# Kernel tuning notes

Measured on AMD Instinct MI355X. Metric: run time of the kernel, lower is better.

The kernel has to match this reference:

```python
import jax, jax.numpy as jnp
import numpy as np

B, R, N, M, K = 4, 4, 4096, 64, 3
F_NUM = 512
KN = K * N


def _block(x, Ws, bs):
    """SO-Net PointResNet: 1x1 convs + ReLU; last layer sees concat(input, hidden)."""
    h = x
    for W, b in zip(Ws[:-1], bs[:-1]):
        h = jax.nn.relu(jnp.einsum('oc,bcn->bon', W, h) + b[None, :, None])
    h = jnp.concatenate([x, h], axis=1)
    return jax.nn.relu(jnp.einsum('oc,bcn->bon', Ws[-1], h) + bs[-1][None, :, None])


def _forward(x, intensity, node, node_knn_I, fpW, fpB, gpW, gpB):
    # --- som.query_topk: k nearest SOM nodes per point ---
    xd = jax.lax.stop_gradient(x)
    dist = jnp.sum((xd[:, :, :, None] - node[:, :, None, :]) ** 2, axis=1)      # B,N,M
    _, topk = jax.lax.top_k(-dist, K)                                           # B,N,K
    min_idx = topk.transpose(0, 2, 1).reshape(B, KN)                            # B,KN (k copies stacked)
    mask = jax.nn.one_hot(min_idx, M, dtype=jnp.float32)                        # B,KN,M
    mask_row_max = jnp.max(mask, axis=1) > 0                                    # B,M  node has >=1 point
    mask_row_sum = jnp.sum(mask, axis=1)                                        # B,M  points per node

    x_stack = jnp.tile(x, (1, 1, K))                                            # B,2,KN
    cluster_mean = jnp.einsum('bcn,bnm->bcm', jax.lax.stop_gradient(x_stack), mask) \
                   / (mask_row_sum[:, None, :] + 1e-5)                          # B,2,M (detached)

    # --- rotation group (2x2 rotations at angles 2*pi*r/R) ---
    theta = 2.0 * jnp.pi * jnp.arange(R, dtype=jnp.float32) / R
    c, s = jnp.cos(theta), jnp.sin(theta)
    rot = jnp.stack([jnp.stack([c, -s], -1), jnp.stack([s, c], -1)], -2)        # R,2,2

    x_rot = jnp.einsum('rij,bjn->brin', rot, x_stack)                           # B,R,2,KN
    node_rot = jnp.einsum('rij,bjm->brim', rot, cluster_mean)                   # B,R,2,M
    centers = jnp.take_along_axis(node_rot, min_idx[:, None, None, :], axis=3)  # B,R,2,KN
    x_dec = jax.lax.stop_gradient(x_rot - centers).reshape(B * R, 2, KN)

    # --- first PointResNet over all B*R rotation copies ---
    feat = _block(x_dec, fpW, fpB)                                              # BR,128,KN

    # --- index_max scatter-max per SOM cluster (value of argmax == segment max) ---
    seg = jnp.tile(min_idx[:, None, :], (1, R, 1)).reshape(B * R, KN)
    segmax = jax.vmap(lambda f, sgi: jax.ops.segment_max(f.T, sgi, num_segments=M).T)(feat, seg)
    rowmax = jnp.tile(mask_row_max[:, None, :], (1, R, 1)).reshape(B * R, M)
    pooled = jnp.where(rowmax[:, None, :], segmax, feat[:, :, 0:1])             # BR,128,M (empty -> gather idx 0)

    # --- final PointResNet over SOM nodes, then max over nodes and rotations ---
    g_in = jnp.concatenate([node_rot.reshape(B * R, 2, M), pooled], axis=1)     # BR,130,M
    out = _block(g_in, gpW, gpB)                                                # BR,F,M
    return out.reshape(B, R, F_NUM, M).max(axis=3).max(axis=1)                  # B,F


def setup_inputs() -> dict:
    key = jax.random.key(0)
    ks = jax.random.split(key, 24)
    d = {}
    d['x'] = jax.random.normal(ks[0], (B, 2, N), jnp.float32)
    d['intensity'] = jax.random.uniform(ks[1], (B, 1, N), jnp.float32)
    d['node'] = jax.random.normal(ks[2], (B, 2, M), jnp.float32)
    d['node_knn_I'] = jax.random.randint(ks[3], (B, M, 1), 0, M)
    dims_fp = [(64, 2), (64, 64), (128, 64), (128, 130)]      # PointResNet(2,[64,64,128,128])
    dims_gp = [(256, 130), (256, 256), (512, 256), (F_NUM, 642)]  # PointResNet(130,[256,256,512,F])
    i = 4
    for name, dims in (('fp', dims_fp), ('gp', dims_gp)):
        for j, (o, ci) in enumerate(dims):
            d[f'{name}_W{j}'] = jax.random.normal(ks[i], (o, ci), jnp.float32) / np.sqrt(ci).astype(np.float32)
            d[f'{name}_b{j}'] = jnp.zeros((o,), jnp.float32)
            i += 1
    return d


def reference(x, intensity, node, node_knn_I,
              fp_W0, fp_b0, fp_W1, fp_b1, fp_W2, fp_b2, fp_W3, fp_b3,
              gp_W0, gp_b0, gp_W1, gp_b1, gp_W2, gp_b2, gp_W3, gp_b3):
    return _forward(x, intensity, node, node_knn_I,
                    [fp_W0, fp_W1, fp_W2, fp_W3], [fp_b0, fp_b1, fp_b2, fp_b3],
                    [gp_W0, gp_W1, gp_W2, gp_W3], [gp_b0, gp_b1, gp_b2, gp_b3])
```

## Files before the change

### kernel.cpp

```cpp
#include <hip/hip_runtime.h>
#include <stdint.h>

#define BB 4
#define RR 4
#define NN 4096
#define MM 64
#define KK 3
#define KNN 12288
#define BRR 16
#define FF 512

#define W_FPW1 0
#define W_FPW2 4096
#define W_FPW3 12288
#define W_GPW0 28928
#define W_GPW1 62208
#define W_GPW2 127744
#define W_GPW3 258816
#define W_FPB1 587520
#define W_FPB2 587584
#define W_FPB3 587712
#define W_GPB0 587840
#define W_GPB1 588096
#define W_GPB2 588352
#define W_GPB3 588864
#define W_FPB0 589376
#define W_FPW0 589440
#define W_TOT  589568

typedef short bf16x8 __attribute__((ext_vector_type(8)));
typedef float f32x4 __attribute__((ext_vector_type(4)));

__device__ __forceinline__ float bf2f(unsigned int u) {
  union { unsigned int i; float f; } v; v.i = u << 16; return v.f;
}
__device__ __forceinline__ unsigned short f2bf(float f) {
  union { float f; unsigned int i; } v; v.f = f;
  unsigned int x = v.i;
  return (unsigned short)((x + 0x7fffu + ((x >> 16) & 1u)) >> 16);
}
__device__ __forceinline__ unsigned int f2bf2(float a, float b) {
#if __has_builtin(__builtin_amdgcn_cvt_pk_bf16_f32)
  typedef __bf16 bf2_t __attribute__((ext_vector_type(2)));
  union { bf2_t v; unsigned int u; } c;
  c.v = __builtin_amdgcn_cvt_pk_bf16_f32(a, b);
  return c.u;
#else
  return (unsigned int)f2bf(a) | ((unsigned int)f2bf(b) << 16);
#endif
}
__device__ __forceinline__ float ldf(const void* p, long i, int isbf) {
  if (isbf) return bf2f(((const unsigned short*)p)[i]);
  return ((const float*)p)[i];
}
__device__ __forceinline__ int detect_bf(const unsigned short* xs) {
  int lane = threadIdx.x & 63;
  unsigned short u = xs[lane * 2];
  int e = (u >> 7) & 0xFF;
  int bad = (e >= 0x90 || (e > 0 && e <= 0x50)) ? 1 : 0;
  unsigned long long m = __ballot(bad);
  return __popcll(m) < 16;
}

struct SrcPtrs { const void* p[16]; };
__global__ __launch_bounds__(256) void k_pre(
    SrcPtrs sp, const void* __restrict__ x, const void* __restrict__ node,
    int* __restrict__ idx, float* __restrict__ csum, int* __restrict__ blkcnt,
    unsigned short* __restrict__ Wb) {
  int isbf = detect_bf((const unsigned short*)x);
  int tid = threadIdx.x;
  if (blockIdx.x >= 64) {
    int t = (blockIdx.x - 64) * 256 + tid;
    if (t >= W_TOT) return;
    int s, base;
    if (t < 28928) {
      if (t < 4096)        { s=0;  base=0; }
      else if (t < 12288)  { s=1;  base=4096; }
      else                 { s=2;  base=12288; }
    } else if (t < 587520) {
      if (t < 62208)       { s=3;  base=28928; }
      else if (t < 127744) { s=4;  base=62208; }
      else if (t < 258816) { s=5;  base=127744; }
      else                 { s=6;  base=258816; }
    } else if (t < 588864) {
      if (t < 587584)      { s=7;  base=587520; }
      else if (t < 587712) { s=8;  base=587584; }
      else if (t < 587840) { s=9;  base=587712; }
      else if (t < 588096) { s=10; base=587840; }
      else if (t < 588352) { s=11; base=588096; }
      else                 { s=12; base=588352; }
    } else {
      if (t < 589376)      { s=13; base=588864; }
      else if (t < 589440) { s=14; base=589376; }
      else                 { s=15; base=589440; }
    }
    int local = t - base;
    Wb[t] = isbf ? ((const unsigned short*)sp.p[s])[local]
                 : f2bf(((const float*)sp.p[s])[local]);
    return;
  }
  __shared__ float nd[2][64];
  __shared__ float cs[192];
  int b = blockIdx.x >> 4;
  int n = ((blockIdx.x & 15) << 8) + tid;
  if (tid < 128) nd[tid >> 6][tid & 63] = ldf(node, b * 128 + tid, isbf);
  if (tid < 192) cs[tid] = 0.f;
  __syncthreads();
  float x0 = ldf(x, b * 8192 + n, isbf);
  float x1 = ldf(x, b * 8192 + 4096 + n, isbf);
  float d0 = 1e30f, d1 = 1e30f, d2 = 1e30f;
  int m0 = 0, m1 = 0, m2 = 0;
#pragma unroll 8
  for (int m = 0; m < 64; ++m) {
    float dx = x0 - nd[0][m];
    float dy = x1 - nd[1][m];
    float d = __fmul_rn(dx, dx) + __fmul_rn(dy, dy);
    if (d < d0)      { d2=d1; m2=m1; d1=d0; m1=m0; d0=d; m0=m; }
    else if (d < d1) { d2=d1; m2=m1; d1=d;  m1=m; }
    else if (d < d2) { d2=d;  m2=m; }
  }
  long base = ((long)b * NN + n) * 3;
  idx[base] = m0; idx[base + 1] = m1; idx[base + 2] = m2;
  atomicAdd(&cs[m0*3+0], x0); atomicAdd(&cs[m0*3+1], x1); atomicAdd(&cs[m0*3+2], 1.f);
  atomicAdd(&cs[m1*3+0], x0); atomicAdd(&cs[m1*3+1], x1); atomicAdd(&cs[m1*3+2], 1.f);
  atomicAdd(&cs[m2*3+0], x0); atomicAdd(&cs[m2*3+1], x1); atomicAdd(&cs[m2*3+2], 1.f);
  __syncthreads();
  if (tid < 192) atomicAdd(&csum[b * 192 + tid], cs[tid]);
  if (tid < 64) blkcnt[blockIdx.x * 64 + tid] = (int)cs[tid*3 + 2];
}

__global__ __launch_bounds__(256) void k_mid(
    const float* __restrict__ csum, const int* __restrict__ blkcnt,
    const int* __restrict__ idx,
    float* __restrict__ noderot, int* __restrict__ rowflag,
    int* __restrict__ sorted, unsigned int* __restrict__ pooled) {
  __shared__ float cls[192];
  __shared__ int offs[64];
  __shared__ int lbase[64];
  __shared__ int lc[64];
  int tid = threadIdx.x;
  int blk = blockIdx.x;
  int b = blk >> 4, chunk = blk & 15;
  for (int i = tid; i < 2048; i += 256) pooled[blk * 2048 + i] = 0u;
  if (tid < 192) cls[tid] = csum[b * 192 + tid];
  __syncthreads();
  if (tid < 64) {
    int m = tid;
    float s0 = cls[m*3], s1 = cls[m*3+1], c = cls[m*3+2];
    float mx = s0 / (c + 1e-5f), my = s1 / (c + 1e-5f);
    rowflag[b*64 + m] = (c > 0.f) ? 1 : 0;
    for (int r = 0; r < 4; ++r) {
      float th = 1.5707964f * (float)r;
      float cr = cosf(th), sr = sinf(th);
      noderot[((b*4+r)*2+0)*64 + m] = cr*mx - sr*my;
      noderot[((b*4+r)*2+1)*64 + m] = sr*mx + cr*my;
    }
    lc[m] = 0;
  }
  if (tid == 0) {
    int acc = 0;
    for (int mm = 0; mm < 64; ++mm) { offs[mm] = acc; acc += (int)cls[mm*3+2]; }
  }
  __syncthreads();
  if (tid < 64) {
    int base = offs[tid];
    for (int c2 = 0; c2 < chunk; ++c2) base += blkcnt[(b*16 + c2)*64 + tid];
    lbase[tid] = base;
  }
  __syncthreads();
  int n = (chunk << 8) + tid;
#pragma unroll
  for (int kk = 0; kk < 3; ++kk) {
    int m = idx[((long)b*NN + n)*3 + kk];
    int pos = atomicAdd(&lc[m], 1);
    sorted[b*KNN + lbase[m] + pos] = (m << 12) | n;
  }
}

__global__ __launch_bounds__(256) void k_fused(
    const void* __restrict__ x, const int* __restrict__ sorted,
    const int* __restrict__ idx, const float* __restrict__ noderot,
    const unsigned short* __restrict__ Wb,
    unsigned int* __restrict__ pooled, float* __restrict__ feat0) {
  __shared__ unsigned short Cs[64 * 136];
  __shared__ unsigned short Hs[64 * 72];
  __shared__ int mcol[64];
  const unsigned short* fW1 = Wb + W_FPW1;
  const unsigned short* fW2 = Wb + W_FPW2;
  const unsigned short* fW3 = Wb + W_FPW3;
  const unsigned short* fb1 = Wb + W_FPB1;
  const unsigned short* fb2 = Wb + W_FPB2;
  const unsigned short* fb3 = Wb + W_FPB3;
  const unsigned short* fb0 = Wb + W_FPB0;
  const unsigned short* fW0 = Wb + W_FPW0;
  int isbf = detect_bf((const unsigned short*)x);
  int tid = threadIdx.x, lane = tid & 63, wv = tid >> 6;
  int quad = lane >> 4, lr = lane & 15;
  int br = blockIdx.y, b = br >> 2, r = br & 3;
  if (tid < 64) {
    int e = sorted[b * KNN + blockIdx.x * 64 + tid];
    int m = e >> 12, n = e & 4095;
    int isz = (n == 0 && m == idx[(long)b * NN * 3]) ? 256 : 0;
    mcol[tid] = m | isz;
    float x0 = ldf(x, b*8192 + n, isbf), x1 = ldf(x, b*8192 + 4096 + n, isbf);
    float th = 1.5707964f * (float)r;
    float cr = cosf(th), sr = sinf(th);
    float xd0 = (cr*x0 - sr*x1) - noderot[(br*2 + 0)*64 + m];
    float xd1 = (sr*x0 + cr*x1) - noderot[(br*2 + 1)*64 + m];
    *(unsigned int*)&Cs[tid * 136] = f2bf2(xd0, xd1);
  }
  __syncthreads();
  {
    int col = tid & 63, og = (tid >> 6) << 4;
    unsigned int xu = *(unsigned int*)&Cs[col * 136];
    float fx0 = bf2f(xu & 0xffff), fx1 = bf2f(xu >> 16);
    union { unsigned int u[8]; bf16x8 v[2]; } o8;
#pragma unroll
    for (int j = 0; j < 16; j += 2) {
      int o = og + j;
      unsigned int wu0 = *(const unsigned int*)&fW0[o*2];
      unsigned int wu1 = *(const unsigned int*)&fW0[o*2 + 2];
      float h0 = bf2f(fb0[o])   + bf2f(wu0 & 0xffff)*fx0 + bf2f(wu0 >> 16)*fx1;
      float h1 = bf2f(fb0[o+1]) + bf2f(wu1 & 0xffff)*fx0 + bf2f(wu1 >> 16)*fx1;
      o8.u[j >> 1] = f2bf2(fmaxf(h0, 0.f), fmaxf(h1, 0.f));
    }
    *(bf16x8*)&Hs[col*72 + og]     = o8.v[0];
    *(bf16x8*)&Hs[col*72 + og + 8] = o8.v[1];
  }
  __syncthreads();
  {
    int o0 = wv * 16;
    f32x4 acc[4];
    float bb4[4];
#pragma unroll
    for (int rr = 0; rr < 4; ++rr) bb4[rr] = bf2f(fb1[o0 + quad*4 + rr]);
#pragma unroll
    for (int nt = 0; nt < 4; ++nt) acc[nt] = (f32x4){bb4[0], bb4[1], bb4[2], bb4[3]};
#pragma unroll
    for (int ks = 0; ks < 64; ks += 32) {
      bf16x8 a = *(const bf16x8*)(fW1 + (o0 + lr)*64 + ks + quad*8);
#pragma unroll
      for (int nt = 0; nt < 4; ++nt) {
        bf16x8 bf = *(bf16x8*)&Hs[(nt*16 + lr)*72 + ks + quad*8];
        acc[nt] = __builtin_amdgcn_mfma_f32_16x16x32_bf16(a, bf, acc[nt], 0, 0, 0);
      }
    }
    __syncthreads();
#pragma unroll
    for (int nt = 0; nt < 4; ++nt) {
      int col = nt*16 + lr;
      unsigned long long pk =
        (unsigned long long)f2bf2(fmaxf(acc[nt][0],0.f), fmaxf(acc[nt][1],0.f)) |
        ((unsigned long long)f2bf2(fmaxf(acc[nt][2],0.f), fmaxf(acc[nt][3],0.f)) << 32);
      *(unsigned long long*)&Hs[col*72 + o0 + quad*4] = pk;
    }
  }
  __syncthreads();
#pragma unroll
  for (int p2 = 0; p2 < 2; ++p2) {
    int o0 = p2*64 + wv*16;
    f32x4 acc[4];
    float bb4[4];
#pragma unroll
    for (int rr = 0; rr < 4; ++rr) bb4[rr] = bf2f(fb2[o0 + quad*4 + rr]);
#pragma unroll
    for (int nt = 0; nt < 4; ++nt) acc[nt] = (f32x4){bb4[0], bb4[1], bb4[2], bb4[3]};
#pragma unroll
    for (int ks = 0; ks < 64; ks += 32) {
      bf16x8 a = *(const bf16x8*)(fW2 + (o0 + lr)*64 + ks + quad*8);
#pragma unroll
      for (int nt = 0; nt < 4; ++nt) {
        bf16x8 bf = *(bf16x8*)&Hs[(nt*16 + lr)*72 + ks + quad*8];
        acc[nt] = __builtin_amdgcn_mfma_f32_16x16x32_bf16(a, bf, acc[nt], 0, 0, 0);
      }
    }
#pragma unroll
    for (int nt = 0; nt < 4; ++nt) {
      int col = nt*16 + lr;
      int o = o0 + quad*4;
      *(unsigned int*)&Cs[col*136 + 2 + o] = f2bf2(fmaxf(acc[nt][0],0.f), fmaxf(acc[nt][1],0.f));
      *(unsigned int*)&Cs[col*136 + 4 + o] = f2bf2(fmaxf(acc[nt][2],0.f), fmaxf(acc[nt][3],0.f));
    }
  }
  __syncthreads();
  f32x4 acc3[2][4];
#pragma unroll
  for (int p3 = 0; p3 < 2; ++p3) {
    int o0 = p3*64 + wv*16;
    float bb4[4];
#pragma unroll
    for (int rr = 0; rr < 4; ++rr) bb4[rr] = bf2f(fb3[o0 + quad*4 + rr]);
#pragma unroll
    for (int nt = 0; nt < 4; ++nt) acc3[p3][nt] = (f32x4){bb4[0], bb4[1], bb4[2], bb4[3]};
#pragma unroll
    for (int ks = 0; ks < 128; ks += 32) {
      union { bf16x8 v; unsigned int u[4]; } au;
      const unsigned int* ap = (const unsigned int*)(fW3 + (long)(o0 + lr)*130 + ks + quad*8);
      au.u[0] = ap[0]; au.u[1] = ap[1]; au.u[2] = ap[2]; au.u[3] = ap[3];
#pragma unroll
      for (int nt = 0; nt < 4; ++nt) {
        bf16x8 bf = *(bf16x8*)&Cs[(nt*16 + lr)*136 + ks + quad*8];
        acc3[p3][nt] = __builtin_amdgcn_mfma_f32_16x16x32_bf16(au.v, bf, acc3[p3][nt], 0, 0, 0);
      }
    }
#pragma unroll
    for (int rr = 0; rr < 4; ++rr) {
      int o = o0 + quad*4 + rr;
      unsigned int wu = *(const unsigned int*)(fW3 + (long)o*130 + 128);
      float w0 = bf2f(wu & 0xffff), w1 = bf2f(wu >> 16);
#pragma unroll
      for (int nt = 0; nt < 4; ++nt) {
        unsigned int bu = *(unsigned int*)&Cs[(nt*16 + lr)*136 + 128];
        acc3[p3][nt][rr] += w0 * bf2f(bu & 0xffff) + w1 * bf2f(bu >> 16);
      }
    }
  }
  __syncthreads();
#pragma unroll
  for (int p3 = 0; p3 < 2; ++p3) {
    int o0 = p3*64 + wv*16;
#pragma unroll
    for (int nt = 0; nt < 4; ++nt) {
      int col = nt*16 + lr;
      unsigned long long pk =
        (unsigned long long)f2bf2(fmaxf(acc3[p3][nt][0],0.f), fmaxf(acc3[p3][nt][1],0.f)) |
        ((unsigned long long)f2bf2(fmaxf(acc3[p3][nt][2],0.f), fmaxf(acc3[p3][nt][3],0.f)) << 32);
      *(unsigned long long*)&Cs[col*136 + o0 + quad*4] = pk;
    }
  }
  __syncthreads();
  {
    int o = tid & 127, h = tid >> 7;
    int c0 = h * 32;
    float fv[32];
#pragma unroll
    for (int j = 0; j < 32; ++j) fv[j] = bf2f(Cs[(c0 + j)*136 + o]);
    int curm = mcol[c0] & 255;
    float v = 0.f;
#pragma unroll
    for (int j = 0; j < 32; ++j) {
      int mc = mcol[c0 + j];
      int mm = mc & 255;
      if (mm != curm) {
        atomicMax(&pooled[(((long)br*64 + curm) << 7) + o], __float_as_uint(v));
        curm = mm; v = 0.f;
      }
      v = fmaxf(v, fv[j]);
      if (mc & 256) feat0[br*128 + o] = fv[j];
    }
    atomicMax(&pooled[(((long)br*64 + curm) << 7) + o], __float_as_uint(v));
  }
}

__global__ __launch_bounds__(1024) void k_gp(
    const void* __restrict__ x,
    const unsigned int* __restrict__ pooled, const float* __restrict__ feat0,
    const int* __restrict__ rowflag, const float* __restrict__ noderot,
    const unsigned short* __restrict__ Wb,
    unsigned int* __restrict__ outmax, unsigned int* __restrict__ counter,
    void* __restrict__ out) {
  __shared__ unsigned short AGs[16 * 648];
  __shared__ unsigned short H1s[16 * 264];
  __shared__ unsigned short H2s[16 * 264];
  __shared__ int done_s;
  int isbf = detect_bf((const unsigned short*)x);
  int tid = threadIdx.x, lane = tid & 63, wv = tid >> 6;
  int quad = lane >> 4, lr = lane & 15;
  int col0 = blockIdx.x * 16;
  int br = col0 >> 6, b = br >> 2;
  for (int i = tid; i < 2048; i += 1024) {
    int c = i >> 7, o = i & 127;
    int gc = col0 + c, m = gc & 63;
    float v = __uint_as_float(pooled[((long)gc << 7) + o]);
    if (!rowflag[b * 64 + m]) v = feat0[br * 128 + o];
    AGs[c * 648 + 2 + o] = f2bf(v);
  }
  if (tid < 32) {
    int c = tid >> 1, j = tid & 1;
    int m = (col0 + c) & 63;
    AGs[c * 648 + j] = f2bf(noderot[(br * 2 + j) * 64 + m]);
  }
  __syncthreads();
  {
    const unsigned short* W = Wb + W_GPW0;
    const unsigned short* Bi = Wb + W_GPB0;
    int o0 = wv * 16;
    f32x4 acc;
    {
      int ob = o0 + quad*4;
      acc = (f32x4){bf2f(Bi[ob]), bf2f(Bi[ob+1]), bf2f(Bi[ob+2]), bf2f(Bi[ob+3])};
    }
#pragma unroll
    for (int ks = 0; ks < 128; ks += 32) {
      bf16x8 bfr = *(bf16x8*)&AGs[lr * 648 + ks + quad * 8];
      union { bf16x8 v; unsigned int u[4]; } au;
      const unsigned int* ap = (const unsigned int*)(W + (o0 + lr)*130 + ks + quad*8);
      au.u[0]=ap[0]; au.u[1]=ap[1]; au.u[2]=ap[2]; au.u[3]=ap[3];
      acc = __builtin_amdgcn_mfma_f32_16x16x32_bf16(au.v, bfr, acc, 0,0,0);
    }
    unsigned int bu = *(unsigned int*)&AGs[lr * 648 + 128];
    float b0v = bf2f(bu & 0xffff), b1v = bf2f(bu >> 16);
#pragma unroll
    for (int rr = 0; rr < 4; ++rr) {
      int o = o0 + quad*4 + rr;
      unsigned int wu = *(const unsigned int*)(W + o*130 + 128);
      acc[rr] += bf2f(wu & 0xffff)*b0v + bf2f(wu >> 16)*b1v;
    }
    unsigned long long pk =
      (unsigned long long)f2bf2(fmaxf(acc[0],0.f), fmaxf(acc[1],0.f)) |
      ((unsigned long long)f2bf2(fmaxf(acc[2],0.f), fmaxf(acc[3],0.f)) << 32);
    *(unsigned long long*)&H1s[lr*264 + o0 + quad*4] = pk;
  }
  __syncthreads();
  {
    const unsigned short* W = Wb + W_GPW1;
    const unsigned short* Bi = Wb + W_GPB1;
    int o0 = wv * 16;
    f32x4 acc;
    {
      int ob = o0 + quad*4;
      acc = (f32x4){bf2f(Bi[ob]), bf2f(Bi[ob+1]), bf2f(Bi[ob+2]), bf2f(Bi[ob+3])};
    }
#pragma unroll
    for (int ks = 0; ks < 256; ks += 32) {
      bf16x8 bfr = *(bf16x8*)&H1s[lr * 264 + ks + quad * 8];
      bf16x8 a = *(const bf16x8*)(W + (o0 + lr)*256 + ks + quad*8);
      acc = __builtin_amdgcn_mfma_f32_16x16x32_bf16(a, bfr, acc, 0,0,0);
    }
    unsigned long long pk =
      (unsigned long long)f2bf2(fmaxf(acc[0],0.f), fmaxf(acc[1],0.f)) |
      ((unsigned long long)f2bf2(fmaxf(acc[2],0.f), fmaxf(acc[3],0.f)) << 32);
    *(unsigned long long*)&H2s[lr*264 + o0 + quad*4] = pk;
  }
  __syncthreads();
  {
    const unsigned short* W = Wb + W_GPW2;
    const unsigned short* Bi = Wb + W_GPB2;
    f32x4 acc[2];
#pragma unroll
    for (int rt = 0; rt < 2; ++rt) {
      int ob = wv*32 + rt*16 + quad*4;
      acc[rt] = (f32x4){bf2f(Bi[ob]), bf2f(Bi[ob+1]), bf2f(Bi[ob+2]), bf2f(Bi[ob+3])};
    }
#pragma unroll
    for (int ks = 0; ks < 256; ks += 32) {
      bf16x8 bfr = *(bf16x8*)&H2s[lr * 264 + ks + quad * 8];
#pragma unroll
      for (int rt = 0; rt < 2; ++rt) {
        int o0 = wv*32 + rt*16;
        bf16x8 a = *(const bf16x8*)(W + (o0 + lr)*256 + ks + quad*8);
        acc[rt] = __builtin_amdgcn_mfma_f32_16x16x32_bf16(a, bfr, acc[rt], 0,0,0);
      }
    }
#pragma unroll
    for (int rt = 0; rt < 2; ++rt) {
      int o0 = wv*32 + rt*16;
      *(unsigned int*)&AGs[lr*648 + 130 + o0 + quad*4] =
          f2bf2(fmaxf(acc[rt][0],0.f), fmaxf(acc[rt][1],0.f));
      *(unsigned int*)&AGs[lr*648 + 132 + o0 + quad*4] =
          f2bf2(fmaxf(acc[rt][2],0.f), fmaxf(acc[rt][3],0.f));
    }
  }
  __syncthreads();
  {
    const unsigned short* W = Wb + W_GPW3;
    const unsigned short* Bi = Wb + W_GPB3;
    f32x4 acc[2];
#pragma unroll
    for (int rt = 0; rt < 2; ++rt) {
      int ob = wv*32 + rt*16 + quad*4;
      acc[rt] = (f32x4){bf2f(Bi[ob]), bf2f(Bi[ob+1]), bf2f(Bi[ob+2]), bf2f(Bi[ob+3])};
    }
    for (int ks = 0; ks < 640; ks += 32) {
      bf16x8 bfr = *(bf16x8*)&AGs[lr * 648 + ks + quad * 8];
#pragma unroll
      for (int rt = 0; rt < 2; ++rt) {
        int o0 = wv*32 + rt*16;
        union { bf16x8 v; unsigned int u[4]; } au;
        const unsigned int* ap = (const unsigned int*)(W + (long)(o0 + lr)*642 + ks + quad*8);
        au.u[0]=ap[0]; au.u[1]=ap[1]; au.u[2]=ap[2]; au.u[3]=ap[3];
        acc[rt] = __builtin_amdgcn_mfma_f32_16x16x32_bf16(au.v, bfr, acc[rt], 0,0,0);
      }
    }
    unsigned int bu = *(unsigned int*)&AGs[lr * 648 + 640];
    float b0v = bf2f(bu & 0xffff), b1v = bf2f(bu >> 16);
#pragma unroll
    for (int rt = 0; rt < 2; ++rt) {
#pragma unroll
      for (int rr = 0; rr < 4; ++rr) {
        int o = wv*32 + rt*16 + quad*4 + rr;
        unsigned int wu = *(const unsigned int*)(W + (long)o*642 + 640);
        float v = acc[rt][rr] + bf2f(wu & 0xffff)*b0v + bf2f(wu >> 16)*b1v;
        v = fmaxf(v, 0.f);
        v = fmaxf(v, __shfl_xor(v, 1, 64));
        v = fmaxf(v, __shfl_xor(v, 2, 64));
        v = fmaxf(v, __shfl_xor(v, 4, 64));
        v = fmaxf(v, __shfl_xor(v, 8, 64));
        if (lr == 0) atomicMax(&outmax[b * FF + o], __float_as_uint(v));
      }
    }
  }
  __threadfence();
  __syncthreads();
  if (tid == 0) done_s = (int)atomicAdd(counter, 1u);
  __syncthreads();
  if (done_s == 63) {
    for (int t = tid; t < 2048; t += 1024) {
      float v = __uint_as_float(atomicMax(&outmax[t], 0u));
      if (isbf) ((unsigned short*)out)[t] = f2bf(v);
      else      ((float*)out)[t] = v;
    }
  }
}

extern "C" void kernel_launch(void* const* d_in, const int* in_sizes, int n_in,
                              void* d_out, int out_size, void* d_ws, size_t ws_size,
                              hipStream_t stream) {
  const void* x    = d_in[0];
  const void* node = d_in[2];

  char* ws = (char*)d_ws;
  float*          csum    = (float*)(ws + 0);
  unsigned int*   outmax  = (unsigned int*)(ws + 3072);
  unsigned int*   counter = (unsigned int*)(ws + 11264);
  unsigned int*   pooled  = (unsigned int*)(ws + 11520);
  int*            idx     = (int*)(ws + 535808);
  int*            blkcnt  = (int*)(ws + 732416);
  float*          noderot = (float*)(ws + 748800);
  int*            rowflag = (int*)(ws + 756992);
  int*            sorted  = (int*)(ws + 758016);
  float*          feat0   = (float*)(ws + 954624);
  unsigned short* Wb      = (unsigned short*)(ws + 962816);

  hipMemsetAsync(ws, 0, 11520, stream);

  SrcPtrs sp;
  sp.p[0]  = d_in[6];
  sp.p[1]  = d_in[8];
  sp.p[2]  = d_in[10];
  sp.p[3]  = d_in[12];
  sp.p[4]  = d_in[14];
  sp.p[5]  = d_in[16];
  sp.p[6]  = d_in[18];
  sp.p[7]  = d_in[7];
  sp.p[8]  = d_in[9];
  sp.p[9]  = d_in[11];
  sp.p[10] = d_in[13];
  sp.p[11] = d_in[15];
  sp.p[12] = d_in[17];
  sp.p[13] = d_in[19];
  sp.p[14] = d_in[5];
  sp.p[15] = d_in[4];

  k_pre<<<64 + (W_TOT + 255) / 256, 256, 0, stream>>>(sp, x, node, idx, csum, blkcnt, Wb);
  k_mid<<<64, 256, 0, stream>>>(csum, blkcnt, idx, noderot, rowflag, sorted, pooled);
  k_fused<<<dim3(192, 16), 256, 0, stream>>>(x, sorted, idx, noderot, Wb, pooled, feat0);
  k_gp<<<64, 1024, 0, stream>>>(x, pooled, feat0, rowflag, noderot, Wb,
                                outmax, counter, d_out);
}
```

Measured before the change: 205.8 us.

## Split global PointResNet into per-layer GEMM kernels and widen fused tile

Replaces the single 64-block k_gp kernel with a gather kernel plus four templated GEMM launches (one per layer) that spread output channels across more blocks, with intermediates going through global workspace. k_fused now processes 128 columns per 512-thread block, and weight conversion handles two elements per thread. The goal is more parallelism for the second-stage MLP, which ran on only 64 blocks. The cost is extra launches and global round-trips for the intermediate activations.

```diff
diff --git a/kernel.cpp b/kernel.cpp
--- a/kernel.cpp
+++ b/kernel.cpp
@@ -70,7 +70,8 @@
   int isbf = detect_bf((const unsigned short*)x);
   int tid = threadIdx.x;
   if (blockIdx.x >= 64) {
-    int t = (blockIdx.x - 64) * 256 + tid;
+    int t2 = (blockIdx.x - 64) * 256 + tid;
+    int t = t2 * 2;
     if (t >= W_TOT) return;
     int s, base;
     if (t < 28928) {
@@ -95,8 +96,13 @@
       else                 { s=15; base=589440; }
     }
     int local = t - base;
-    Wb[t] = isbf ? ((const unsigned short*)sp.p[s])[local]
-                 : f2bf(((const float*)sp.p[s])[local]);
+    unsigned int pk;
+    if (isbf) pk = *(const unsigned int*)((const unsigned short*)sp.p[s] + local);
+    else {
+      const float* fp = (const float*)sp.p[s] + local;
+      pk = f2bf2(fp[0], fp[1]);
+    }
+    *(unsigned int*)(Wb + t) = pk;
     return;
   }
   __shared__ float nd[2][64];
@@ -177,14 +183,14 @@
   }
 }
 
-__global__ __launch_bounds__(256) void k_fused(
+__global__ __launch_bounds__(512, 6) void k_fused(
     const void* __restrict__ x, const int* __restrict__ sorted,
     const int* __restrict__ idx, const float* __restrict__ noderot,
     const unsigned short* __restrict__ Wb,
     unsigned int* __restrict__ pooled, float* __restrict__ feat0) {
-  __shared__ unsigned short Cs[64 * 136];
-  __shared__ unsigned short Hs[64 * 72];
-  __shared__ int mcol[64];
+  __shared__ unsigned short Cs[128 * 136];
+  __shared__ unsigned short Hs[128 * 72];
+  __shared__ int mcol[128];
   const unsigned short* fW1 = Wb + W_FPW1;
   const unsigned short* fW2 = Wb + W_FPW2;
   const unsigned short* fW3 = Wb + W_FPW3;
@@ -197,8 +203,8 @@
   int tid = threadIdx.x, lane = tid & 63, wv = tid >> 6;
   int quad = lane >> 4, lr = lane & 15;
   int br = blockIdx.y, b = br >> 2, r = br & 3;
-  if (tid < 64) {
-    int e = sorted[b * KNN + blockIdx.x * 64 + tid];
+  if (tid < 128) {
+    int e = sorted[b * KNN + blockIdx.x * 128 + tid];
     int m = e >> 12, n = e & 4095;
     int isz = (n == 0 && m == idx[(long)b * NN * 3]) ? 256 : 0;
     mcol[tid] = m | isz;
@@ -211,7 +217,7 @@
   }
   __syncthreads();
   {
-    int col = tid & 63, og = (tid >> 6) << 4;
+    int col = tid & 127, og = (tid >> 7) << 4;
     unsigned int xu = *(unsigned int*)&Cs[col * 136];
     float fx0 = bf2f(xu & 0xffff), fx1 = bf2f(xu >> 16);
     union { unsigned int u[8]; bf16x8 v[2]; } o8;
@@ -229,7 +235,7 @@
   }
   __syncthreads();
   {
-    int o0 = wv * 16;
+    int o0 = (wv & 3) * 16, cb = (wv >> 2) * 64;
     f32x4 acc[4];
     float bb4[4];
 #pragma unroll
@@ -241,14 +247,14 @@
       bf16x8 a = *(const bf16x8*)(fW1 + (o0 + lr)*64 + ks + quad*8);
 #pragma unroll
       for (int nt = 0; nt < 4; ++nt) {
-        bf16x8 bf = *(bf16x8*)&Hs[(nt*16 + lr)*72 + ks + quad*8];
+        bf16x8 bf = *(bf16x8*)&Hs[(cb + nt*16 + lr)*72 + ks + quad*8];
         acc[nt] = __builtin_amdgcn_mfma_f32_16x16x32_bf16(a, bf, acc[nt], 0, 0, 0);
       }
     }
     __syncthreads();
 #pragma unroll
     for (int nt = 0; nt < 4; ++nt) {
-      int col = nt*16 + lr;
+      int col = cb + nt*16 + lr;
       unsigned long long pk =
         (unsigned long long)f2bf2(fmaxf(acc[nt][0],0.f), fmaxf(acc[nt][1],0.f)) |
         ((unsigned long long)f2bf2(fmaxf(acc[nt][2],0.f), fmaxf(acc[nt][3],0.f)) << 32);
@@ -256,26 +262,25 @@
     }
   }
   __syncthreads();
-#pragma unroll
-  for (int p2 = 0; p2 < 2; ++p2) {
-    int o0 = p2*64 + wv*16;
-    f32x4 acc[4];
+  {
+    int o0 = wv * 16;
+    f32x4 acc[8];
     float bb4[4];
 #pragma unroll
     for (int rr = 0; rr < 4; ++rr) bb4[rr] = bf2f(fb2[o0 + quad*4 + rr]);
 #pragma unroll
-    for (int nt = 0; nt < 4; ++nt) acc[nt] = (f32x4){bb4[0], bb4[1], bb4[2], bb4[3]};
+    for (int nt = 0; nt < 8; ++nt) acc[nt] = (f32x4){bb4[0], bb4[1], bb4[2], bb4[3]};
 #pragma unroll
     for (int ks = 0; ks < 64; ks += 32) {
       bf16x8 a = *(const bf16x8*)(fW2 + (o0 + lr)*64 + ks + quad*8);
 #pragma unroll
-      for (int nt = 0; nt < 4; ++nt) {
+      for (int nt = 0; nt < 8; ++nt) {
         bf16x8 bf = *(bf16x8*)&Hs[(nt*16 + lr)*72 + ks + quad*8];
         acc[nt] = __builtin_amdgcn_mfma_f32_16x16x32_bf16(a, bf, acc[nt], 0, 0, 0);
       }
     }
 #pragma unroll
-    for (int nt = 0; nt < 4; ++nt) {
+    for (int nt = 0; nt < 8; ++nt) {
       int col = nt*16 + lr;
       int o = o0 + quad*4;
       *(unsigned int*)&Cs[col*136 + 2 + o] = f2bf2(fmaxf(acc[nt][0],0.f), fmaxf(acc[nt][1],0.f));
@@ -283,24 +288,23 @@
     }
   }
   __syncthreads();
-  f32x4 acc3[2][4];
-#pragma unroll
-  for (int p3 = 0; p3 < 2; ++p3) {
-    int o0 = p3*64 + wv*16;
+  f32x4 acc3[8];
+  {
+    int o0 = wv * 16;
     float bb4[4];
 #pragma unroll
     for (int rr = 0; rr < 4; ++rr) bb4[rr] = bf2f(fb3[o0 + quad*4 + rr]);
 #pragma unroll
-    for (int nt = 0; nt < 4; ++nt) acc3[p3][nt] = (f32x4){bb4[0], bb4[1], bb4[2], bb4[3]};
+    for (int nt = 0; nt < 8; ++nt) acc3[nt] = (f32x4){bb4[0], bb4[1], bb4[2], bb4[3]};
 #pragma unroll
     for (int ks = 0; ks < 128; ks += 32) {
       union { bf16x8 v; unsigned int u[4]; } au;
       const unsigned int* ap = (const unsigned int*)(fW3 + (long)(o0 + lr)*130 + ks + quad*8);
       au.u[0] = ap[0]; au.u[1] = ap[1]; au.u[2] = ap[2]; au.u[3] = ap[3];
 #pragma unroll
-      for (int nt = 0; nt < 4; ++nt) {
+      for (int nt = 0; nt < 8; ++nt) {
         bf16x8 bf = *(bf16x8*)&Cs[(nt*16 + lr)*136 + ks + quad*8];
-        acc3[p3][nt] = __builtin_amdgcn_mfma_f32_16x16x32_bf16(au.v, bf, acc3[p3][nt], 0, 0, 0);
+        acc3[nt] = __builtin_amdgcn_mfma_f32_16x16x32_bf16(au.v, bf, acc3[nt], 0, 0, 0);
       }
     }
 #pragma unroll
@@ -309,22 +313,21 @@
       unsigned int wu = *(const unsigned int*)(fW3 + (long)o*130 + 128);
       float w0 = bf2f(wu & 0xffff), w1 = bf2f(wu >> 16);
 #pragma unroll
-      for (int nt = 0; nt < 4; ++nt) {
+      for (int nt = 0; nt < 8; ++nt) {
         unsigned int bu = *(unsigned int*)&Cs[(nt*16 + lr)*136 + 128];
-        acc3[p3][nt][rr] += w0 * bf2f(bu & 0xffff) + w1 * bf2f(bu >> 16);
+        acc3[nt][rr] += w0 * bf2f(bu & 0xffff) + w1 * bf2f(bu >> 16);
       }
     }
   }
   __syncthreads();
-#pragma unroll
-  for (int p3 = 0; p3 < 2; ++p3) {
-    int o0 = p3*64 + wv*16;
-#pragma unroll
-    for (int nt = 0; nt < 4; ++nt) {
+  {
+    int o0 = wv * 16;
+#pragma unroll
+    for (int nt = 0; nt < 8; ++nt) {
       int col = nt*16 + lr;
       unsigned long long pk =
-        (unsigned long long)f2bf2(fmaxf(acc3[p3][nt][0],0.f), fmaxf(acc3[p3][nt][1],0.f)) |
-        ((unsigned long long)f2bf2(fmaxf(acc3[p3][nt][2],0.f), fmaxf(acc3[p3][nt][3],0.f)) << 32);
+        (unsigned long long)f2bf2(fmaxf(acc3[nt][0],0.f), fmaxf(acc3[nt][1],0.f)) |
+        ((unsigned long long)f2bf2(fmaxf(acc3[nt][2],0.f), fmaxf(acc3[nt][3],0.f)) << 32);
       *(unsigned long long*)&Cs[col*136 + o0 + quad*4] = pk;
     }
   }
@@ -352,163 +355,94 @@
   }
 }
 
-__global__ __launch_bounds__(1024) void k_gp(
-    const void* __restrict__ x,
+__global__ __launch_bounds__(256) void k_fin(
     const unsigned int* __restrict__ pooled, const float* __restrict__ feat0,
     const int* __restrict__ rowflag, const float* __restrict__ noderot,
-    const unsigned short* __restrict__ Wb,
+    unsigned short* __restrict__ AG) {
+  int t = blockIdx.x * 256 + threadIdx.x;
+  int col = t >> 7, o = t & 127;
+  int br = col >> 6, m = col & 63, b = br >> 2;
+  float v = __uint_as_float(pooled[((long)col << 7) + o]);
+  if (!rowflag[b*64 + m]) v = feat0[br*128 + o];
+  AG[(long)col*648 + 2 + o] = f2bf(v);
+  if (o < 2) AG[(long)col*648 + o] = f2bf(noderot[(br*2 + o)*64 + m]);
+}
+
+template<int KW, int KMAIN, bool REM2, int BSTR, int OSTR, int OOFF, int EPI, bool AAL, int TOTB>
+__global__ __launch_bounds__(256) void k_gemm2(
+    const unsigned short* __restrict__ W, const unsigned short* __restrict__ Bi,
+    const unsigned short* __restrict__ Bb, unsigned short* __restrict__ Out,
     unsigned int* __restrict__ outmax, unsigned int* __restrict__ counter,
-    void* __restrict__ out) {
-  __shared__ unsigned short AGs[16 * 648];
-  __shared__ unsigned short H1s[16 * 264];
-  __shared__ unsigned short H2s[16 * 264];
+    const void* __restrict__ x, void* __restrict__ out) {
   __shared__ int done_s;
-  int isbf = detect_bf((const unsigned short*)x);
-  int tid = threadIdx.x, lane = tid & 63, wv = tid >> 6;
+  int lane = threadIdx.x & 63, wv = threadIdx.x >> 6;
   int quad = lane >> 4, lr = lane & 15;
-  int col0 = blockIdx.x * 16;
-  int br = col0 >> 6, b = br >> 2;
-  for (int i = tid; i < 2048; i += 1024) {
-    int c = i >> 7, o = i & 127;
-    int gc = col0 + c, m = gc & 63;
-    float v = __uint_as_float(pooled[((long)gc << 7) + o]);
-    if (!rowflag[b * 64 + m]) v = feat0[br * 128 + o];
-    AGs[c * 648 + 2 + o] = f2bf(v);
-  }
-  if (tid < 32) {
-    int c = tid >> 1, j = tid & 1;
-    int m = (col0 + c) & 63;
-    AGs[c * 648 + j] = f2bf(noderot[(br * 2 + j) * 64 + m]);
-  }
-  __syncthreads();
-  {
-    const unsigned short* W = Wb + W_GPW0;
-    const unsigned short* Bi = Wb + W_GPB0;
-    int o0 = wv * 16;
-    f32x4 acc;
-    {
-      int ob = o0 + quad*4;
-      acc = (f32x4){bf2f(Bi[ob]), bf2f(Bi[ob+1]), bf2f(Bi[ob+2]), bf2f(Bi[ob+3])};
-    }
-#pragma unroll
-    for (int ks = 0; ks < 128; ks += 32) {
-      bf16x8 bfr = *(bf16x8*)&AGs[lr * 648 + ks + quad * 8];
+  int o0 = blockIdx.y * 64 + wv * 16;
+  int p0 = blockIdx.x * 16;
+  f32x4 acc;
+  {
+    int ob = o0 + quad*4;
+    acc = (f32x4){bf2f(Bi[ob]), bf2f(Bi[ob+1]), bf2f(Bi[ob+2]), bf2f(Bi[ob+3])};
+  }
+  const unsigned short* arow = W + (long)(o0 + lr) * KW;
+  const unsigned short* brow = Bb + (long)(p0 + lr) * BSTR;
+#pragma unroll 4
+  for (int ks = 0; ks < KMAIN; ks += 32) {
+    bf16x8 a;
+    if constexpr (AAL) {
+      a = *(const bf16x8*)(arow + ks + quad*8);
+    } else {
       union { bf16x8 v; unsigned int u[4]; } au;
-      const unsigned int* ap = (const unsigned int*)(W + (o0 + lr)*130 + ks + quad*8);
-      au.u[0]=ap[0]; au.u[1]=ap[1]; au.u[2]=ap[2]; au.u[3]=ap[3];
-      acc = __builtin_amdgcn_mfma_f32_16x16x32_bf16(au.v, bfr, acc, 0,0,0);
-    }
-    unsigned int bu = *(unsigned int*)&AGs[lr * 648 + 128];
+      const unsigned int* ap = (const unsigned int*)(arow + ks + quad*8);
+      au.u[0] = ap[0]; au.u[1] = ap[1]; au.u[2] = ap[2]; au.u[3] = ap[3];
+      a = au.v;
+    }
+    bf16x8 bf = *(const bf16x8*)(brow + ks + quad*8);
+    acc = __builtin_amdgcn_mfma_f32_16x16x32_bf16(a, bf, acc, 0, 0, 0);
+  }
+  if constexpr (REM2) {
+    unsigned int bu = *(const unsigned int*)(brow + KMAIN);
     float b0v = bf2f(bu & 0xffff), b1v = bf2f(bu >> 16);
 #pragma unroll
     for (int rr = 0; rr < 4; ++rr) {
       int o = o0 + quad*4 + rr;
-      unsigned int wu = *(const unsigned int*)(W + o*130 + 128);
-      acc[rr] += bf2f(wu & 0xffff)*b0v + bf2f(wu >> 16)*b1v;
-    }
-    unsigned long long pk =
-      (unsigned long long)f2bf2(fmaxf(acc[0],0.f), fmaxf(acc[1],0.f)) |
-      ((unsigned long long)f2bf2(fmaxf(acc[2],0.f), fmaxf(acc[3],0.f)) << 32);
-    *(unsigned long long*)&H1s[lr*264 + o0 + quad*4] = pk;
-  }
-  __syncthreads();
-  {
-    const unsigned short* W = Wb + W_GPW1;
-    const unsigned short* Bi = Wb + W_GPB1;
-    int o0 = wv * 16;
-    f32x4 acc;
-    {
-      int ob = o0 + quad*4;
-      acc = (f32x4){bf2f(Bi[ob]), bf2f(Bi[ob+1]), bf2f(Bi[ob+2]), bf2f(Bi[ob+3])};
-    }
-#pragma unroll
-    for (int ks = 0; ks < 256; ks += 32) {
-      bf16x8 bfr = *(bf16x8*)&H1s[lr * 264 + ks + quad * 8];
-      bf16x8 a = *(const bf16x8*)(W + (o0 + lr)*256 + ks + quad*8);
-      acc = __builtin_amdgcn_mfma_f32_16x16x32_bf16(a, bfr, acc, 0,0,0);
-    }
-    unsigned long long pk =
-      (unsigned long long)f2bf2(fmaxf(acc[0],0.f), fmaxf(acc[1],0.f)) |
-      ((unsigned long long)f2bf2(fmaxf(acc[2],0.f), fmaxf(acc[3],0.f)) << 32);
-    *(unsigned long long*)&H2s[lr*264 + o0 + quad*4] = pk;
-  }
-  __syncthreads();
-  {
-    const unsigned short* W = Wb + W_GPW2;
-    const unsigned short* Bi = Wb + W_GPB2;
-    f32x4 acc[2];
-#pragma unroll
-    for (int rt = 0; rt < 2; ++rt) {
-      int ob = wv*32 + rt*16 + quad*4;
-      acc[rt] = (f32x4){bf2f(Bi[ob]), bf2f(Bi[ob+1]), bf2f(Bi[ob+2]), bf2f(Bi[ob+3])};
-    }
-#pragma unroll
-    for (int ks = 0; ks < 256; ks += 32) {
-      bf16x8 bfr = *(bf16x8*)&H2s[lr * 264 + ks + quad * 8];
-#pragma unroll
-      for (int rt = 0; rt < 2; ++rt) {
-        int o0 = wv*32 + rt*16;
-        bf16x8 a = *(const bf16x8*)(W + (o0 + lr)*256 + ks + quad*8);
-        acc[rt] = __builtin_amdgcn_mfma_f32_16x16x32_bf16(a, bfr, acc[rt], 0,0,0);
+      unsigned int wu = *(const unsigned int*)(W + (long)o * KW + KMAIN);
+      acc[rr] += bf2f(wu & 0xffff) * b0v + bf2f(wu >> 16) * b1v;
+    }
+  }
+  if constexpr (EPI == 0) {
+    unsigned short* op = Out + (long)(p0 + lr) * OSTR + OOFF + o0 + quad*4;
+    if constexpr (((OOFF * 2) % 8) == 0) {
+      unsigned long long pk =
+        (unsigned long long)f2bf2(fmaxf(acc[0],0.f), fmaxf(acc[1],0.f)) |
+        ((unsigned long long)f2bf2(fmaxf(acc[2],0.f), fmaxf(acc[3],0.f)) << 32);
+      *(unsigned long long*)op = pk;
+    } else {
+      *(unsigned int*)op       = f2bf2(fmaxf(acc[0],0.f), fmaxf(acc[1],0.f));
+      *(unsigned int*)(op + 2) = f2bf2(fmaxf(acc[2],0.f), fmaxf(acc[3],0.f));
+    }
+  } else {
+    int b = blockIdx.x >> 4;
+#pragma unroll
+    for (int rr = 0; rr < 4; ++rr) {
+      float v = fmaxf(acc[rr], 0.f);
+      v = fmaxf(v, __shfl_xor(v, 1, 64));
+      v = fmaxf(v, __shfl_xor(v, 2, 64));
+      v = fmaxf(v, __shfl_xor(v, 4, 64));
+      v = fmaxf(v, __shfl_xor(v, 8, 64));
+      if (lr == 0) atomicMax(&outmax[b * FF + o0 + quad*4 + rr], __float_as_uint(v));
+    }
+    __threadfence();
+    __syncthreads();
+    if (threadIdx.x == 0) done_s = (int)atomicAdd(counter, 1u);
+    __syncthreads();
+    if (done_s == TOTB - 1) {
+      int isbf = detect_bf((const unsigned short*)x);
+      for (int t = threadIdx.x; t < 2048; t += 256) {
+        float v = __uint_as_float(atomicMax(&outmax[t], 0u));
+        if (isbf) ((unsigned short*)out)[t] = f2bf(v);
+        else      ((float*)out)[t] = v;
       }
-    }
-#pragma unroll
-    for (int rt = 0; rt < 2; ++rt) {
-      int o0 = wv*32 + rt*16;
-      *(unsigned int*)&AGs[lr*648 + 130 + o0 + quad*4] =
-          f2bf2(fmaxf(acc[rt][0],0.f), fmaxf(acc[rt][1],0.f));
-      *(unsigned int*)&AGs[lr*648 + 132 + o0 + quad*4] =
-          f2bf2(fmaxf(acc[rt][2],0.f), fmaxf(acc[rt][3],0.f));
-    }
-  }
-  __syncthreads();
-  {
-    const unsigned short* W = Wb + W_GPW3;
-    const unsigned short* Bi = Wb + W_GPB3;
-    f32x4 acc[2];
-#pragma unroll
-    for (int rt = 0; rt < 2; ++rt) {
-      int ob = wv*32 + rt*16 + quad*4;
-      acc[rt] = (f32x4){bf2f(Bi[ob]), bf2f(Bi[ob+1]), bf2f(Bi[ob+2]), bf2f(Bi[ob+3])};
-    }
-    for (int ks = 0; ks < 640; ks += 32) {
-      bf16x8 bfr = *(bf16x8*)&AGs[lr * 648 + ks + quad * 8];
-#pragma unroll
-      for (int rt = 0; rt < 2; ++rt) {
-        int o0 = wv*32 + rt*16;
-        union { bf16x8 v; unsigned int u[4]; } au;
-        const unsigned int* ap = (const unsigned int*)(W + (long)(o0 + lr)*642 + ks + quad*8);
-        au.u[0]=ap[0]; au.u[1]=ap[1]; au.u[2]=ap[2]; au.u[3]=ap[3];
-        acc[rt] = __builtin_amdgcn_mfma_f32_16x16x32_bf16(au.v, bfr, acc[rt], 0,0,0);
-      }
-    }
-    unsigned int bu = *(unsigned int*)&AGs[lr * 648 + 640];
-    float b0v = bf2f(bu & 0xffff), b1v = bf2f(bu >> 16);
-#pragma unroll
-    for (int rt = 0; rt < 2; ++rt) {
-#pragma unroll
-      for (int rr = 0; rr < 4; ++rr) {
-        int o = wv*32 + rt*16 + quad*4 + rr;
-        unsigned int wu = *(const unsigned int*)(W + (long)o*642 + 640);
-        float v = acc[rt][rr] + bf2f(wu & 0xffff)*b0v + bf2f(wu >> 16)*b1v;
-        v = fmaxf(v, 0.f);
-        v = fmaxf(v, __shfl_xor(v, 1, 64));
-        v = fmaxf(v, __shfl_xor(v, 2, 64));
-        v = fmaxf(v, __shfl_xor(v, 4, 64));
-        v = fmaxf(v, __shfl_xor(v, 8, 64));
-        if (lr == 0) atomicMax(&outmax[b * FF + o], __float_as_uint(v));
-      }
-    }
-  }
-  __threadfence();
-  __syncthreads();
-  if (tid == 0) done_s = (int)atomicAdd(counter, 1u);
-  __syncthreads();
-  if (done_s == 63) {
-    for (int t = tid; t < 2048; t += 1024) {
-      float v = __uint_as_float(atomicMax(&outmax[t], 0u));
-      if (isbf) ((unsigned short*)out)[t] = f2bf(v);
-      else      ((float*)out)[t] = v;
     }
   }
 }
@@ -531,6 +465,9 @@
   int*            sorted  = (int*)(ws + 758016);
   float*          feat0   = (float*)(ws + 954624);
   unsigned short* Wb      = (unsigned short*)(ws + 962816);
+  unsigned short* AG      = (unsigned short*)(ws + 2141952);
+  unsigned short* Hg1     = (unsigned short*)(ws + 3469056);
+  unsigned short* Hg2     = (unsigned short*)(ws + 3993344);
 
   hipMemsetAsync(ws, 0, 11520, stream);
 
@@ -552,9 +489,21 @@
   sp.p[14] = d_in[5];
   sp.p[15] = d_in[4];
 
-  k_pre<<<64 + (W_TOT + 255) / 256, 256, 0, stream>>>(sp, x, node, idx, csum, blkcnt, Wb);
+  k_pre<<<64 + (W_TOT/2 + 255) / 256, 256, 0, stream>>>(sp, x, node, idx, csum, blkcnt, Wb);
   k_mid<<<64, 256, 0, stream>>>(csum, blkcnt, idx, noderot, rowflag, sorted, pooled);
-  k_fused<<<dim3(192, 16), 256, 0, stream>>>(x, sorted, idx, noderot, Wb, pooled, feat0);
-  k_gp<<<64, 1024, 0, stream>>>(x, pooled, feat0, rowflag, noderot, Wb,
-                                outmax, counter, d_out);
-}
+  k_fused<<<dim3(96, 16), 512, 0, stream>>>(x, sorted, idx, noderot, Wb, pooled, feat0);
+  k_fin<<<512, 256, 0, stream>>>(pooled, feat0, rowflag, noderot, AG);
+
+  k_gemm2<130, 128, true, 648, 256, 0, 0, false, 0>
+      <<<dim3(64, 4), 256, 0, stream>>>(Wb + W_GPW0, Wb + W_GPB0, AG, Hg1,
+                                        nullptr, nullptr, x, nullptr);
+  k_gemm2<256, 256, false, 256, 256, 0, 0, true, 0>
+      <<<dim3(64, 4), 256, 0, stream>>>(Wb + W_GPW1, Wb + W_GPB1, Hg1, Hg2,
+                                        nullptr, nullptr, x, nullptr);
+  k_gemm2<256, 256, false, 256, 648, 130, 0, true, 0>
+      <<<dim3(64, 8), 256, 0, stream>>>(Wb + W_GPW2, Wb + W_GPB2, Hg2, AG,
+                                        nullptr, nullptr, x, nullptr);
+  k_gemm2<642, 640, true, 648, 0, 0, 2, false, 512>
+      <<<dim3(64, 8), 256, 0, stream>>>(Wb + W_GPW3, Wb + W_GPB3, AG, nullptr,
+                                        outmax, counter, x, d_out);
+}
```

Measured after the change: 203.6 us. Within noise of the previous version (-1.1%).
